# Kernel optimization log

Hardware: AMD Instinct MI355X
Metric: run time of the kernel (lower is better)

Reference implementation:

```python
import jax, jax.numpy as jnp
import numpy as np

V, E = 100000, 128   # vocab, embed_size
B, S, N = 32, 1024, 16  # batch, seq_len, n_negatives


def setup_inputs() -> dict:
    key = jax.random.key(0)
    k1, k2, k3, k4 = jax.random.split(key, 4)
    sentence = jax.random.randint(k1, (B, S), 0, V, dtype=jnp.int64)
    context = jax.random.normal(k2, (B, S, E), dtype=jnp.float32)
    # WalkerAlias negative sampling happens on CPU in the original; here the
    # sampled indices are precomputed inputs (uniform counter ** power -> uniform).
    neg_samples = jax.random.randint(k3, (B, S, N), 0, V, dtype=jnp.int64)
    W = jax.random.normal(k4, (V, E), dtype=jnp.float32) * 0.02
    return {"sentence": sentence, "context": context, "neg_samples": neg_samples, "W": W}


def reference(sentence, context, neg_samples, W):
    emb = W[sentence]                                   # [B,S,E] gather
    pos_loss = jax.nn.log_sigmoid(jnp.sum(emb * context, axis=-1))          # [B,S]
    neg_emb = W[neg_samples]                            # [B,S,N,E] gather
    neg_scores = jnp.einsum('bsne,bse->bsn', neg_emb, context)              # [B,S,N]
    neg_loss = jnp.sum(jax.nn.log_sigmoid(-neg_scores), axis=-1)            # [B,S]
    return -jnp.sum(pos_loss + neg_loss)
```

## Files before the change

kernel.cpp:

```cpp
#include <hip/hip_runtime.h>
#include <hip/hip_bf16.h>
#include <cmath>

#define NS_ROWS    32768
#define NS_NEG     16
#define NS_TARGETS 17
#define NS_TILE    15
#define NS_CPAD    132

__device__ __forceinline__ float log_sigmoid_f(float x) {
    return fminf(x, 0.0f) - log1pf(__expf(-fabsf(x)));
}

__global__ __launch_bounds__(1024) void neg_sampling_kernel(
    const int*   __restrict__ sentence,
    const float* __restrict__ context,
    const int*   __restrict__ neg,
    const float* __restrict__ W,
    float*       __restrict__ out)
{
    __shared__ float cctx[NS_TILE][NS_CPAD];
    __shared__ float wsum[16];

    const int tid     = threadIdx.x;
    const int rowbase = blockIdx.x * NS_TILE;

    const int group = tid >> 2;
    const int sub   = tid & 3;
    const int lrow  = group / NS_TARGETS;
    const int tgt   = group - lrow * NS_TARGETS;
    const int row   = rowbase + lrow;
    const bool active = (lrow < NS_TILE) && (row < NS_ROWS);

    float4 w0, w1, w2, w3, w4, w5, w6, w7;
    if (active) {
        const int idx = (tgt == 0) ? sentence[row] : neg[row * NS_NEG + (tgt - 1)];
        const float4* __restrict__ wr =
            reinterpret_cast<const float4*>(W) + (size_t)idx * 32 + sub;
        w0 = wr[0];  w1 = wr[4];  w2 = wr[8];  w3 = wr[12];
        w4 = wr[16]; w5 = wr[20]; w6 = wr[24]; w7 = wr[28];
    } else {
        w0=w1=w2=w3=w4=w5=w6=w7 = make_float4(0.f,0.f,0.f,0.f);
    }

    if (tid < NS_TILE * 32) {
        const int r  = tid >> 5;
        const int e4 = tid & 31;
        const int grow = rowbase + r;
        if (grow < NS_ROWS) {
            const float4 v = reinterpret_cast<const float4*>(context)[grow * 32 + e4];
            *reinterpret_cast<float4*>(&cctx[r][e4 * 4]) = v;
        }
    }
    __syncthreads();

    float loss = 0.0f;
    if (active) {
        const float* crow = &cctx[lrow][0];
        float acc = 0.0f;
        {
            float4 c;
            c = *reinterpret_cast<const float4*>(crow + (sub +  0) * 4);
            acc += w0.x*c.x + w0.y*c.y + w0.z*c.z + w0.w*c.w;
            c = *reinterpret_cast<const float4*>(crow + (sub +  4) * 4);
            acc += w1.x*c.x + w1.y*c.y + w1.z*c.z + w1.w*c.w;
            c = *reinterpret_cast<const float4*>(crow + (sub +  8) * 4);
            acc += w2.x*c.x + w2.y*c.y + w2.z*c.z + w2.w*c.w;
            c = *reinterpret_cast<const float4*>(crow + (sub + 12) * 4);
            acc += w3.x*c.x + w3.y*c.y + w3.z*c.z + w3.w*c.w;
            c = *reinterpret_cast<const float4*>(crow + (sub + 16) * 4);
            acc += w4.x*c.x + w4.y*c.y + w4.z*c.z + w4.w*c.w;
            c = *reinterpret_cast<const float4*>(crow + (sub + 20) * 4);
            acc += w5.x*c.x + w5.y*c.y + w5.z*c.z + w5.w*c.w;
            c = *reinterpret_cast<const float4*>(crow + (sub + 24) * 4);
            acc += w6.x*c.x + w6.y*c.y + w6.z*c.z + w6.w*c.w;
            c = *reinterpret_cast<const float4*>(crow + (sub + 28) * 4);
            acc += w7.x*c.x + w7.y*c.y + w7.z*c.z + w7.w*c.w;
        }
        acc += __shfl_xor(acc, 1, 64);
        acc += __shfl_xor(acc, 2, 64);
        if (sub == 0) {
            loss = log_sigmoid_f((tgt == 0) ? acc : -acc);
        }
    }

#pragma unroll
    for (int m = 32; m >= 1; m >>= 1) loss += __shfl_xor(loss, m, 64);

    const int wave = tid >> 6, lane = tid & 63;
    if (lane == 0) wsum[wave] = loss;
    __syncthreads();
    if (tid == 0) {
        float t = 0.0f;
#pragma unroll
        for (int i = 0; i < 16; ++i) t += wsum[i];
        atomicAdd(out, -t);
    }
}

extern "C" void kernel_launch(void* const* d_in, const int* in_sizes, int n_in,
                              void* d_out, int out_size, void* d_ws, size_t ws_size,
                              hipStream_t stream) {
    const int*   sentence = (const int*)d_in[0];
    const float* context  = (const float*)d_in[1];
    const int*   neg      = (const int*)d_in[2];
    const float* W        = (const float*)d_in[3];
    float*       out      = (float*)d_out;

    hipMemsetAsync(out, 0, sizeof(float), stream);

    const int blocks = (NS_ROWS + NS_TILE - 1) / NS_TILE;
    neg_sampling_kernel<<<blocks, 1024, 0, stream>>>(sentence, context, neg, W, out);
}
```

Before: 51.89 us.

## Convert embedding table to bf16 in workspace before gathering rows

Adds a pre-pass that converts the whole fp32 embedding table W to bf16 in the workspace. The main kernel then gathers half-size rows and widens them to fp32 for the dot products. The intent is to halve the bytes moved by the random row gathers. In exchange, every call reads the full 51 MB table and writes 25.6 MB, which is far more traffic than the roughly 35 MB the gathers touch, and the bf16 rounding adds error. The fp32 path is kept as a fallback for when the workspace is too small.

```diff
diff --git a/kernel.cpp b/kernel.cpp
--- a/kernel.cpp
+++ b/kernel.cpp
@@ -7,12 +7,116 @@
 #define NS_TARGETS 17
 #define NS_TILE    15
 #define NS_CPAD    132
+#define NS_V       100000
+#define NS_E       128
+
+typedef unsigned short u16;
+typedef u16 u16x8 __attribute__((ext_vector_type(8)));
 
 __device__ __forceinline__ float log_sigmoid_f(float x) {
     return fminf(x, 0.0f) - log1pf(__expf(-fabsf(x)));
 }
 
-__global__ __launch_bounds__(1024) void neg_sampling_kernel(
+__device__ __forceinline__ u16 f32_to_bf16_rne(float f) {
+    union { float f; unsigned u; } v; v.f = f;
+    const unsigned u = v.u + (0x7fffu + ((v.u >> 16) & 1u));
+    return (u16)(u >> 16);
+}
+__device__ __forceinline__ float bf16_to_f32(u16 h) {
+    union { unsigned u; float f; } v; v.u = ((unsigned)h) << 16;
+    return v.f;
+}
+
+__global__ __launch_bounds__(256) void ns_convert_kernel(
+    const float* __restrict__ W, u16* __restrict__ Wbf)
+{
+    const size_t base = ((size_t)blockIdx.x * 256 + threadIdx.x) * 8;
+    if (base >= (size_t)NS_V * NS_E) return;
+    const float4 a = *reinterpret_cast<const float4*>(W + base);
+    const float4 b = *reinterpret_cast<const float4*>(W + base + 4);
+    u16x8 o;
+    o[0]=f32_to_bf16_rne(a.x); o[1]=f32_to_bf16_rne(a.y);
+    o[2]=f32_to_bf16_rne(a.z); o[3]=f32_to_bf16_rne(a.w);
+    o[4]=f32_to_bf16_rne(b.x); o[5]=f32_to_bf16_rne(b.y);
+    o[6]=f32_to_bf16_rne(b.z); o[7]=f32_to_bf16_rne(b.w);
+    *reinterpret_cast<u16x8*>(Wbf + base) = o;
+}
+
+__global__ __launch_bounds__(1024) void ns_main_bf16_kernel(
+    const int*   __restrict__ sentence,
+    const float* __restrict__ context,
+    const int*   __restrict__ neg,
+    const u16*   __restrict__ Wbf,
+    float*       __restrict__ out)
+{
+    __shared__ float cctx[NS_TILE][NS_CPAD];
+    __shared__ float wsum[16];
+
+    const int tid     = threadIdx.x;
+    const int rowbase = blockIdx.x * NS_TILE;
+
+    const int group = tid >> 2;
+    const int sub   = tid & 3;
+    const int lrow  = group / NS_TARGETS;
+    const int tgt   = group - lrow * NS_TARGETS;
+    const int row   = rowbase + lrow;
+    const bool active = (lrow < NS_TILE) && (row < NS_ROWS);
+
+    u16x8 g0, g1, g2, g3;
+    if (active) {
+        const int idx = (tgt == 0) ? sentence[row] : neg[(row << 4) + (tgt - 1)];
+        const u16x8* __restrict__ wr =
+            reinterpret_cast<const u16x8*>(Wbf + (size_t)idx * NS_E) + sub;
+        g0 = wr[0]; g1 = wr[4]; g2 = wr[8]; g3 = wr[12];
+    } else {
+        g0 = g1 = g2 = g3 = (u16x8)0;
+    }
+
+    if (tid < NS_TILE * 32) {
+        const int r = tid >> 5, e4 = tid & 31;
+        const int grow = rowbase + r;
+        if (grow < NS_ROWS) {
+            const float4 v = reinterpret_cast<const float4*>(context)[grow * 32 + e4];
+            *reinterpret_cast<float4*>(&cctx[r][e4 * 4]) = v;
+        }
+    }
+    __syncthreads();
+
+    float loss = 0.0f;
+    if (active) {
+        const float4* cr = reinterpret_cast<const float4*>(&cctx[lrow][0]);
+        float acc = 0.0f;
+#define NS_CHUNK(g, k)                                                        \
+        {                                                                     \
+            const float4 ca = cr[2 * sub + 8 * (k)];                          \
+            const float4 cb = cr[2 * sub + 8 * (k) + 1];                      \
+            acc += bf16_to_f32(g[0]) * ca.x + bf16_to_f32(g[1]) * ca.y        \
+                 + bf16_to_f32(g[2]) * ca.z + bf16_to_f32(g[3]) * ca.w        \
+                 + bf16_to_f32(g[4]) * cb.x + bf16_to_f32(g[5]) * cb.y        \
+                 + bf16_to_f32(g[6]) * cb.z + bf16_to_f32(g[7]) * cb.w;       \
+        }
+        NS_CHUNK(g0, 0) NS_CHUNK(g1, 1) NS_CHUNK(g2, 2) NS_CHUNK(g3, 3)
+#undef NS_CHUNK
+        acc += __shfl_xor(acc, 1, 64);
+        acc += __shfl_xor(acc, 2, 64);
+        if (sub == 0) loss = log_sigmoid_f((tgt == 0) ? acc : -acc);
+    }
+
+#pragma unroll
+    for (int m = 32; m >= 1; m >>= 1) loss += __shfl_xor(loss, m, 64);
+
+    const int wave = tid >> 6, lane = tid & 63;
+    if (lane == 0) wsum[wave] = loss;
+    __syncthreads();
+    if (tid == 0) {
+        float t = 0.0f;
+#pragma unroll
+        for (int i = 0; i < 16; ++i) t += wsum[i];
+        atomicAdd(out, -t);
+    }
+}
+
+__global__ __launch_bounds__(1024) void ns_main_f32_kernel(
     const int*   __restrict__ sentence,
     const float* __restrict__ context,
     const int*   __restrict__ neg,
@@ -24,7 +128,6 @@
 
     const int tid     = threadIdx.x;
     const int rowbase = blockIdx.x * NS_TILE;
-
     const int group = tid >> 2;
     const int sub   = tid & 3;
     const int lrow  = group / NS_TARGETS;
@@ -34,7 +137,7 @@
 
     float4 w0, w1, w2, w3, w4, w5, w6, w7;
     if (active) {
-        const int idx = (tgt == 0) ? sentence[row] : neg[row * NS_NEG + (tgt - 1)];
+        const int idx = (tgt == 0) ? sentence[row] : neg[(row << 4) + (tgt - 1)];
         const float4* __restrict__ wr =
             reinterpret_cast<const float4*>(W) + (size_t)idx * 32 + sub;
         w0 = wr[0];  w1 = wr[4];  w2 = wr[8];  w3 = wr[12];
@@ -44,8 +147,7 @@
     }
 
     if (tid < NS_TILE * 32) {
-        const int r  = tid >> 5;
-        const int e4 = tid & 31;
+        const int r = tid >> 5, e4 = tid & 31;
         const int grow = rowbase + r;
         if (grow < NS_ROWS) {
             const float4 v = reinterpret_cast<const float4*>(context)[grow * 32 + e4];
@@ -56,32 +158,19 @@
 
     float loss = 0.0f;
     if (active) {
-        const float* crow = &cctx[lrow][0];
-        float acc = 0.0f;
-        {
-            float4 c;
-            c = *reinterpret_cast<const float4*>(crow + (sub +  0) * 4);
-            acc += w0.x*c.x + w0.y*c.y + w0.z*c.z + w0.w*c.w;
-            c = *reinterpret_cast<const float4*>(crow + (sub +  4) * 4);
-            acc += w1.x*c.x + w1.y*c.y + w1.z*c.z + w1.w*c.w;
-            c = *reinterpret_cast<const float4*>(crow + (sub +  8) * 4);
-            acc += w2.x*c.x + w2.y*c.y + w2.z*c.z + w2.w*c.w;
-            c = *reinterpret_cast<const float4*>(crow + (sub + 12) * 4);
-            acc += w3.x*c.x + w3.y*c.y + w3.z*c.z + w3.w*c.w;
-            c = *reinterpret_cast<const float4*>(crow + (sub + 16) * 4);
-            acc += w4.x*c.x + w4.y*c.y + w4.z*c.z + w4.w*c.w;
-            c = *reinterpret_cast<const float4*>(crow + (sub + 20) * 4);
-            acc += w5.x*c.x + w5.y*c.y + w5.z*c.z + w5.w*c.w;
-            c = *reinterpret_cast<const float4*>(crow + (sub + 24) * 4);
-            acc += w6.x*c.x + w6.y*c.y + w6.z*c.z + w6.w*c.w;
-            c = *reinterpret_cast<const float4*>(crow + (sub + 28) * 4);
-            acc += w7.x*c.x + w7.y*c.y + w7.z*c.z + w7.w*c.w;
-        }
+        const float4* cr = reinterpret_cast<const float4*>(&cctx[lrow][0]);
+        float acc;
+        acc  = w0.x*cr[sub+ 0].x + w0.y*cr[sub+ 0].y + w0.z*cr[sub+ 0].z + w0.w*cr[sub+ 0].w;
+        acc += w1.x*cr[sub+ 4].x + w1.y*cr[sub+ 4].y + w1.z*cr[sub+ 4].z + w1.w*cr[sub+ 4].w;
+        acc += w2.x*cr[sub+ 8].x + w2.y*cr[sub+ 8].y + w2.z*cr[sub+ 8].z + w2.w*cr[sub+ 8].w;
+        acc += w3.x*cr[sub+12].x + w3.y*cr[sub+12].y + w3.z*cr[sub+12].z + w3.w*cr[sub+12].w;
+        acc += w4.x*cr[sub+16].x + w4.y*cr[sub+16].y + w4.z*cr[sub+16].z + w4.w*cr[sub+16].w;
+        acc += w5.x*cr[sub+20].x + w5.y*cr[sub+20].y + w5.z*cr[sub+20].z + w5.w*cr[sub+20].w;
+        acc += w6.x*cr[sub+24].x + w6.y*cr[sub+24].y + w6.z*cr[sub+24].z + w6.w*cr[sub+24].w;
+        acc += w7.x*cr[sub+28].x + w7.y*cr[sub+28].y + w7.z*cr[sub+28].z + w7.w*cr[sub+28].w;
         acc += __shfl_xor(acc, 1, 64);
         acc += __shfl_xor(acc, 2, 64);
-        if (sub == 0) {
-            loss = log_sigmoid_f((tgt == 0) ? acc : -acc);
-        }
+        if (sub == 0) loss = log_sigmoid_f((tgt == 0) ? acc : -acc);
     }
 
 #pragma unroll
@@ -110,5 +199,14 @@
     hipMemsetAsync(out, 0, sizeof(float), stream);
 
     const int blocks = (NS_ROWS + NS_TILE - 1) / NS_TILE;
-    neg_sampling_kernel<<<blocks, 1024, 0, stream>>>(sentence, context, neg, W, out);
-}
+    const size_t need = (size_t)NS_V * NS_E * sizeof(u16);
+
+    if (ws_size >= need) {
+        u16* Wbf = (u16*)d_ws;
+        const int cblocks = (NS_V * NS_E / 8 + 255) / 256;
+        ns_convert_kernel<<<cblocks, 256, 0, stream>>>(W, Wbf);
+        ns_main_bf16_kernel<<<blocks, 1024, 0, stream>>>(sentence, context, neg, Wbf, out);
+    } else {
+        ns_main_f32_kernel<<<blocks, 1024, 0, stream>>>(sentence, context, neg, W, out);
+    }
+}
```

Result: slower. 58.19 us (+12.2%).
